# Performance work log

Hardware: AMD Instinct MI355X
Metric: run time of the kernel (lower is better)

The kernel has to match this reference:

```python
import jax, jax.numpy as jnp
import numpy as np

B, S, D = 4, 4096, 1024
DD = 4 * D
N_EXPERTS = 8
CAPACITY = 1.0
LN_EPS = 1e-5


def setup_inputs() -> dict:
    key = jax.random.key(0)
    ks = jax.random.split(key, 8)
    s1 = 1.0 / np.sqrt(D)
    s2 = 1.0 / np.sqrt(DD)
    return {
        "x": jax.random.normal(ks[0], (B, S, D), jnp.float32),
        "gate_w": jax.random.normal(ks[1], (N_EXPERTS, D), jnp.float32) * 0.02,
        "ln_w": jnp.ones((D,), jnp.float32),
        "ln_b": jnp.zeros((D,), jnp.float32),
        "fc1s": jax.random.normal(ks[2], (N_EXPERTS, DD, D), jnp.float32) * s1,
        "b1s": jax.random.normal(ks[3], (N_EXPERTS, DD), jnp.float32) * s1,
        "fc2s": jax.random.normal(ks[4], (N_EXPERTS, D, DD), jnp.float32) * s2,
        "b2s": jax.random.normal(ks[5], (N_EXPERTS, D), jnp.float32) * s2,
    }


def reference(x, gate_w, ln_w, ln_b, fc1s, b1s, fc2s, b2s):
    og_shape = x.shape
    d = og_shape[-1]
    xf = x.reshape(-1, d)                       # (bs, d)
    bs = xf.shape[0]
    n = gate_w.shape[0]
    k = int(bs * CAPACITY) // n                 # static capacity per expert

    # softmax gating over experts
    scores = jax.nn.softmax(xf @ gate_w.T, axis=-1)   # (bs, n)

    # per-expert top-k tokens (column-wise descending sort, take first k)
    vals, idx = jax.lax.top_k(scores.T, k)      # (n, k)
    kept_w = vals.T                              # (k, n)
    kept_idx = idx.T                             # (k, n)
    flat_idx = kept_idx.reshape(-1)              # (k*n,) row-major: k outer, n inner

    # gather selected tokens, layernorm
    y = xf[flat_idx].reshape(k, n, d)            # (k, n, d)
    mu = y.mean(-1, keepdims=True)
    var = ((y - mu) ** 2).mean(-1, keepdims=True)
    y = (y - mu) * jax.lax.rsqrt(var + LN_EPS) * ln_w + ln_b

    # per-expert grouped GEMMs
    h = jnp.einsum('knd,nfd->knf', y, fc1s) + b1s          # (k, n, dd)
    h = jax.nn.gelu(h, approximate=True)                   # tanh gelu
    out = jnp.einsum('knf,ndf->knd', h, fc2s) + b2s        # (k, n, d)

    # weight by gate scores and scatter-add back onto the input tokens
    out = out * kept_w[..., None]
    xf = xf.at[flat_idx].add(out.reshape(k * n, d))
    return xf.reshape(og_shape)
```

## Files before the change

kernel.cpp:

```cpp
#include <hip/hip_runtime.h>

#define TOK  16384
#define NEXP 8
#define DIM  1024
#define DDIM 4096
#define KCAP 2048

typedef float  floatx4 __attribute__((ext_vector_type(4)));
typedef short  shortx8 __attribute__((ext_vector_type(8)));

static __device__ __forceinline__ unsigned short f2bf(float x) {
  unsigned u = __float_as_uint(x);
  return (unsigned short)((u + 0x7fffu + ((u >> 16) & 1u)) >> 16);
}

__global__ __launch_bounds__(256) void cvt_kernel(const float* __restrict__ src,
                                                  unsigned short* __restrict__ dst, int n4) {
  int i = blockIdx.x * 256 + threadIdx.x;
  if (i < n4) {
    float4 v = ((const float4*)src)[i];
    ushort4 o = make_ushort4(f2bf(v.x), f2bf(v.y), f2bf(v.z), f2bf(v.w));
    ((ushort4*)dst)[i] = o;
  }
}

__global__ __launch_bounds__(256) void gate_kernel(const float* __restrict__ x,
                                                   const float* __restrict__ gw,
                                                   float* __restrict__ scores) {
  __shared__ float gws[NEXP * DIM];
  int tid = threadIdx.x;
  for (int i = tid; i < NEXP * DIM / 4; i += 256)
    ((float4*)gws)[i] = ((const float4*)gw)[i];
  __syncthreads();
  int wave = tid >> 6, lane = tid & 63;
  int t = blockIdx.x * 4 + wave;
  const float4* xr = (const float4*)(x + (size_t)t * DIM);
  float4 xv[4];
#pragma unroll
  for (int j = 0; j < 4; ++j) xv[j] = xr[j * 64 + lane];
  float acc[NEXP];
#pragma unroll
  for (int e = 0; e < NEXP; ++e) acc[e] = 0.f;
#pragma unroll
  for (int e = 0; e < NEXP; ++e) {
    const float4* g4 = (const float4*)(gws + e * DIM);
#pragma unroll
    for (int j = 0; j < 4; ++j) {
      float4 g = g4[j * 64 + lane];
      acc[e] += xv[j].x * g.x + xv[j].y * g.y + xv[j].z * g.z + xv[j].w * g.w;
    }
  }
#pragma unroll
  for (int off = 32; off > 0; off >>= 1) {
#pragma unroll
    for (int e = 0; e < NEXP; ++e) acc[e] += __shfl_down(acc[e], off);
  }
  if (lane == 0) {
    float mx = acc[0];
#pragma unroll
    for (int e = 1; e < NEXP; ++e) mx = fmaxf(mx, acc[e]);
    float ex[NEXP], sum = 0.f;
#pragma unroll
    for (int e = 0; e < NEXP; ++e) { ex[e] = expf(acc[e] - mx); sum += ex[e]; }
    float inv = 1.f / sum;
#pragma unroll
    for (int e = 0; e < NEXP; ++e) scores[(size_t)e * TOK + t] = ex[e] * inv;
  }
}

#define TKT 1024
#define TKW (TKT / 64)

__device__ __forceinline__ void walk_suffix(const int* hist, int nbins, int cnt_in,
                                            int tid, int* shOut) {
  if (tid < 64) {
    int lane = tid;
    int cum = 0;
    for (int g = nbins / 64 - 1; g >= 0; --g) {
      int c = hist[g * 64 + lane];
      int s = c;
#pragma unroll
      for (int off = 1; off < 64; off <<= 1) {
        int o = __shfl_down(s, off);
        if (lane + off < 64) s += o;
      }
      int gs = __shfl(s, 0);
      if (cnt_in + cum + gs >= KCAP) {
        unsigned long long m = __ballot(cnt_in + cum + s >= KCAP);
        int l = 63 - __clzll(m);
        int sAt = __shfl(s, l), cAt = __shfl(c, l);
        if (lane == 0) { shOut[0] = g * 64 + l; shOut[1] = cnt_in + cum + sAt - cAt; }
        break;
      }
      cum += gs;
    }
  }
}

__global__ __launch_bounds__(TKT) void topk_kernel(const float* __restrict__ scores,
                                                   int* __restrict__ sel,
                                                   float* __restrict__ selw) {
  int e = blockIdx.x;
  const float* s = scores + (size_t)e * TOK;
  int tid = threadIdx.x, lane = tid & 63, wave = tid >> 6;
  __shared__ int hist[2048];
  __shared__ int shBin[2];
  __shared__ int wsum[TKW];

  for (int i = tid; i < 2048; i += TKT) hist[i] = 0;
  __syncthreads();
  for (int i = tid; i < TOK; i += TKT)
    atomicAdd(&hist[__float_as_uint(s[i]) >> 21], 1);
  __syncthreads();
  walk_suffix(hist, 2048, 0, tid, shBin);
  __syncthreads();
  unsigned bin1 = (unsigned)shBin[0];
  int cab = shBin[1];
  __syncthreads();

  for (int i = tid; i < 2048; i += TKT) hist[i] = 0;
  __syncthreads();
  for (int i = tid; i < TOK; i += TKT) {
    unsigned v = __float_as_uint(s[i]);
    if ((v >> 21) == bin1) atomicAdd(&hist[(v >> 10) & 0x7FFu], 1);
  }
  __syncthreads();
  walk_suffix(hist, 2048, cab, tid, shBin);
  __syncthreads();
  unsigned pre21 = (bin1 << 11) | (unsigned)shBin[0];
  cab = shBin[1];
  __syncthreads();

  for (int i = tid; i < 1024; i += TKT) hist[i] = 0;
  __syncthreads();
  for (int i = tid; i < TOK; i += TKT) {
    unsigned v = __float_as_uint(s[i]);
    if ((v >> 10) == pre21) atomicAdd(&hist[v & 0x3FFu], 1);
  }
  __syncthreads();
  walk_suffix(hist, 1024, cab, tid, shBin);
  __syncthreads();
  unsigned T = (pre21 << 10) | (unsigned)shBin[0];
  int n_gt = shBin[1];
  int need = KCAP - n_gt;

  __shared__ int pos;
  __shared__ int tiebase;
  if (tid == 0) { pos = 0; tiebase = 0; }
  __syncthreads();
  for (int chunk = 0; chunk < TOK; chunk += TKT) {
    int i = chunk + tid;
    unsigned v = __float_as_uint(s[i]);
    if (v > T) {
      int p = atomicAdd(&pos, 1);
      sel[e * KCAP + p]  = i;
      selw[e * KCAP + p] = __uint_as_float(v);
    }
    bool tie = (v == T);
    unsigned long long m = __ballot(tie);
    if (lane == 0) wsum[wave] = __popcll(m);
    __syncthreads();
    int base = tiebase;
    for (int w = 0; w < wave; ++w) base += wsum[w];
    int rank = base + __popcll(m & ((1ull << lane) - 1ull));
    if (tie && rank < need) {
      sel[e * KCAP + n_gt + rank]  = i;
      selw[e * KCAP + n_gt + rank] = __uint_as_float(T);
    }
    __syncthreads();
    if (tid == 0) {
      int tb = 0;
#pragma unroll
      for (int w = 0; w < TKW; ++w) tb += wsum[w];
      tiebase += tb;
    }
    __syncthreads();
  }
}

__global__ __launch_bounds__(256) void gather_ln_kernel(const float* __restrict__ x,
                                                        const int* __restrict__ sel,
                                                        const float* __restrict__ lnw,
                                                        const float* __restrict__ lnb,
                                                        unsigned short* __restrict__ Y) {
  int e = blockIdx.y, i = blockIdx.x;
  int tid = threadIdx.x, lane = tid & 63, wave = tid >> 6;
  int t = sel[e * KCAP + i];
  const float4* xr = (const float4*)(x + (size_t)t * DIM);
  float4 v = xr[tid];
  float s  = v.x + v.y + v.z + v.w;
  float sq = v.x * v.x + v.y * v.y + v.z * v.z + v.w * v.w;
#pragma unroll
  for (int off = 32; off > 0; off >>= 1) { s += __shfl_down(s, off); sq += __shfl_down(sq, off); }
  __shared__ float red[8];
  if (lane == 0) { red[wave] = s; red[4 + wave] = sq; }
  __syncthreads();
  s  = red[0] + red[1] + red[2] + red[3];
  sq = red[4] + red[5] + red[6] + red[7];
  float mu  = s * (1.f / DIM);
  float var = sq * (1.f / DIM) - mu * mu;
  float rs  = rsqrtf(var + 1e-5f);
  float4 w = ((const float4*)lnw)[tid];
  float4 b = ((const float4*)lnb)[tid];
  ushort4 o = make_ushort4(f2bf((v.x - mu) * rs * w.x + b.x),
                           f2bf((v.y - mu) * rs * w.y + b.y),
                           f2bf((v.z - mu) * rs * w.z + b.z),
                           f2bf((v.w - mu) * rs * w.w + b.w));
  ((ushort4*)(Y + ((size_t)e * KCAP + i) * DIM))[tid] = o;
}

#define BM  256
#define BN  256
#define BKT 64
#define HTILE 8192

template <int MODE, int M, int N, int K>
__global__ __launch_bounds__(512, 2) void gemm_kernel(
    const unsigned short* __restrict__ Aall,
    const unsigned short* __restrict__ Ball,
    const float* __restrict__ biasAll,
    unsigned short* __restrict__ Hall,
    float* __restrict__ Out,
    const int* __restrict__ sel, const float* __restrict__ selw) {

  __shared__ __align__(16) unsigned short As[2 * 2 * HTILE];
  __shared__ __align__(16) unsigned short Bs[2 * 2 * HTILE];
  __shared__ int   selS[BM];
  __shared__ float wS[BM];

  int tid = threadIdx.x, lane = tid & 63, wave = tid >> 6;
  int m_w = wave >> 2, n_w = wave & 3;
  int hb  = n_w >> 1, nb0 = (n_w & 1) * 64;
  int row = lane & 15, quad = lane >> 4, r7 = row & 7;
  int r8 = lane >> 3, j8 = lane & 7;

  constexpr int nxt = N >> 8, nyt = M >> 8, per = nxt * nyt;
  constexpr int nwg = per * NEXP;
  int bid = blockIdx.x;
  int swz = (bid & 7) * (nwg >> 3) + (bid >> 3);
  int e   = swz / per;
  int rem = swz - e * per;
  int by  = rem / nxt;
  int bx  = rem - by * nxt;
  int m0 = by * BM, n0 = bx * BN;
  constexpr int NT = K / BKT;

  const unsigned short* A = Aall + (size_t)e * M * K;
  const unsigned short* B = Ball + (size_t)e * N * K;
  const float* bias = biasAll + (size_t)e * N;

  if (MODE == 2 && tid < BM) {
    selS[tid] = sel[e * KCAP + m0 + tid];
    wS[tid]   = selw[e * KCAP + m0 + tid];
  }
  __syncthreads();

#define STAGE(DST, G, RC0, TT, HALF, BUF)                                              \
  do {                                                                                 \
    int tt_ = (TT) < NT ? (TT) : NT - 1;                                               \
    const unsigned short* g_ =                                                         \
        (G) + (size_t)((RC0) + (HALF) * 128 + wave * 16 + r8) * K + tt_ * BKT +        \
        ((j8 ^ r8) << 3);                                                              \
    unsigned short* l_ = (DST) + ((BUF) * 2 + (HALF)) * HTILE + wave * 16 * 64;        \
    __builtin_amdgcn_global_load_lds((const __attribute__((address_space(1))) void*)g_,\
        (__attribute__((address_space(3))) void*)l_, 16, 0, 0);                        \
    __builtin_amdgcn_global_load_lds(                                                  \
        (const __attribute__((address_space(1))) void*)(g_ + (size_t)8 * K),           \
        (__attribute__((address_space(3))) void*)(l_ + 8 * 64), 16, 0, 0);             \
  } while (0)

#define LDA(MQ)                                                                        \
  _Pragma("unroll") for (int ti = 0; ti < 4; ++ti)                                     \
  _Pragma("unroll") for (int kki = 0; kki < 2; ++kki)                                  \
    a[ti][kki] = *(const shortx8*)&As[(cur * 2 + m_w) * HTILE +                        \
        ((MQ) * 64 + ti * 16 + row) * 64 + (((quad + 4 * kki) ^ r7) << 3)];

#define LDB(BREG, NQ)                                                                  \
  _Pragma("unroll") for (int tj = 0; tj < 2; ++tj)                                     \
  _Pragma("unroll") for (int kki = 0; kki < 2; ++kki)                                  \
    BREG[tj][kki] = *(const shortx8*)&Bs[(cur * 2 + hb) * HTILE +                      \
        (nb0 + (NQ) * 32 + tj * 16 + row) * 64 + (((quad + 4 * kki) ^ r7) << 3)];

#define MFMAQ(MQ, BREG, NQ)                                                            \
  _Pragma("unroll") for (int kki = 0; kki < 2; ++kki)                                  \
  _Pragma("unroll") for (int ti = 0; ti < 4; ++ti)                                     \
  _Pragma("unroll") for (int tj = 0; tj < 2; ++tj)                                     \
    acc[(MQ) * 4 + ti][(NQ) * 2 + tj] = __builtin_amdgcn_mfma_f32_16x16x32_bf16(       \
        a[ti][kki], BREG[tj][kki], acc[(MQ) * 4 + ti][(NQ) * 2 + tj], 0, 0, 0);

#define PH_MID()                                                                       \
  __builtin_amdgcn_s_barrier();                                                        \
  asm volatile("s_waitcnt lgkmcnt(0)" ::: "memory");                                   \
  __builtin_amdgcn_s_setprio(1);

#define PH_END()                                                                       \
  __builtin_amdgcn_s_setprio(0);                                                       \
  __builtin_amdgcn_s_barrier();

#define PH_END_VM(NN)                                                                  \
  __builtin_amdgcn_s_setprio(0);                                                       \
  asm volatile("s_waitcnt vmcnt(" #NN ")" ::: "memory");                               \
  __builtin_amdgcn_s_barrier();

  floatx4 acc[8][4];
  floatx4 zero = {0.f, 0.f, 0.f, 0.f};
#pragma unroll
  for (int i = 0; i < 8; ++i)
#pragma unroll
    for (int j = 0; j < 4; ++j) acc[i][j] = zero;

  shortx8 a[4][2], b0[2][2], b1[2][2];

  STAGE(As, A, m0, 0, 0, 0);
  STAGE(Bs, B, n0, 0, 0, 0);
  STAGE(As, A, m0, 0, 1, 0);
  STAGE(Bs, B, n0, 0, 1, 0);
  STAGE(As, A, m0, 1, 0, 1);
  STAGE(Bs, B, n0, 1, 0, 1);
  asm volatile("s_waitcnt vmcnt(4)" ::: "memory");
  __builtin_amdgcn_s_barrier();

  for (int t = 0; t < NT; ++t) {
    int cur = t & 1, nb = cur ^ 1;
    LDA(0); LDB(b0, 0);
    STAGE(As, A, m0, t + 1, 1, nb);
    STAGE(Bs, B, n0, t + 1, 1, nb);
    asm volatile("s_waitcnt lgkmcnt(8)" ::: "memory");
    PH_MID(); MFMAQ(0, b0, 0); PH_END();
    LDB(b1, 1);
    PH_MID(); MFMAQ(0, b1, 1); PH_END();
    LDA(1);
    PH_MID(); MFMAQ(1, b0, 0); PH_END();
    STAGE(As, A, m0, t + 2, 0, cur);
    STAGE(Bs, B, n0, t + 2, 0, cur);
    PH_MID(); MFMAQ(1, b1, 1); PH_END_VM(4);
  }
  asm volatile("s_waitcnt vmcnt(0)" ::: "memory");

#pragma unroll
  for (int ti = 0; ti < 8; ++ti) {
#pragma unroll
    for (int tj = 0; tj < 4; ++tj) {
      int gn = n0 + n_w * 64 + tj * 16 + row;
      float bb = bias[gn];
#pragma unroll
      for (int r = 0; r < 4; ++r) {
        int lrow = m_w * 128 + ti * 16 + quad * 4 + r;
        float v = acc[ti][tj][r] + bb;
        if (MODE == 1) {
          float u = 0.7978845608028654f * (v + 0.044715f * v * v * v);
          u = fminf(u, 15.f);
          float e2 = __expf(2.f * u);
          float th = __fdividef(e2 - 1.f, e2 + 1.f);
          float g = 0.5f * v * (1.f + th);
          Hall[(size_t)e * M * N + (size_t)(m0 + lrow) * N + gn] = f2bf(g);
        } else {
          atomicAdd(&Out[(size_t)selS[lrow] * DIM + gn], wS[lrow] * v);
        }
      }
    }
  }
#undef STAGE
#undef LDA
#undef LDB
#undef MFMAQ
#undef PH_MID
#undef PH_END
#undef PH_END_VM
}

extern "C" void kernel_launch(void* const* d_in, const int* in_sizes, int n_in,
                              void* d_out, int out_size, void* d_ws, size_t ws_size,
                              hipStream_t stream) {
  const float* x   = (const float*)d_in[0];
  const float* gw  = (const float*)d_in[1];
  const float* lnw = (const float*)d_in[2];
  const float* lnb = (const float*)d_in[3];
  const float* fc1 = (const float*)d_in[4];
  const float* b1  = (const float*)d_in[5];
  const float* fc2 = (const float*)d_in[6];
  const float* b2  = (const float*)d_in[7];
  float* out = (float*)d_out;

  char* p = (char*)d_ws;
  float* scores = (float*)p;                 p += (size_t)NEXP * TOK * 4;
  int*   sel    = (int*)p;                   p += (size_t)NEXP * KCAP * 4;
  float* selw   = (float*)p;                 p += (size_t)NEXP * KCAP * 4;
  unsigned short* Wb = (unsigned short*)p;   p += (size_t)NEXP * DDIM * DIM * 2;
  unsigned short* Y  = (unsigned short*)p;   p += (size_t)NEXP * KCAP * DIM * 2;
  unsigned short* H  = (unsigned short*)p;   p += (size_t)NEXP * KCAP * DDIM * 2;

  hipMemcpyAsync(out, x, (size_t)TOK * DIM * sizeof(float), hipMemcpyDeviceToDevice, stream);

  gate_kernel<<<TOK / 4, 256, 0, stream>>>(x, gw, scores);
  topk_kernel<<<NEXP, TKT, 0, stream>>>(scores, sel, selw);
  gather_ln_kernel<<<dim3(KCAP, NEXP), 256, 0, stream>>>(x, sel, lnw, lnb, Y);

  const int n4w = NEXP * DDIM * DIM / 4;
  cvt_kernel<<<n4w / 256, 256, 0, stream>>>(fc1, Wb, n4w);
  gemm_kernel<1, KCAP, DDIM, DIM><<<dim3((DDIM / BN) * (KCAP / BM) * NEXP), 512, 0, stream>>>(
      Y, Wb, b1, H, nullptr, nullptr, nullptr);

  cvt_kernel<<<n4w / 256, 256, 0, stream>>>(fc2, Wb, n4w);
  gemm_kernel<2, KCAP, DIM, DDIM><<<dim3((DIM / BN) * (KCAP / BM) * NEXP), 512, 0, stream>>>(
      H, Wb, b2, nullptr, out, sel, selw);
}
```

Baseline: 826.8 us.

## Fold input copy into gate kernel and reschedule GEMM prefetch stages

The gate kernel now writes the input rows straight to the output buffer, which removes the separate device-to-device memcpy. The GEMM prefetch order changes so the B tile for step t+1 is issued in two halves interleaved between MFMA phases, with the waitcnt thresholds adjusted to match. The MFMA loop order moves kki innermost. M/N/K become runtime arguments instead of template constants, which may cost some compile-time constant folding of index math and the K-loop trip count. The new waitcnt accounting is fragile and could open a race if the counts no longer match the outstanding loads.

```diff
diff --git a/kernel.cpp b/kernel.cpp
--- a/kernel.cpp
+++ b/kernel.cpp
@@ -26,7 +26,8 @@
 
 __global__ __launch_bounds__(256) void gate_kernel(const float* __restrict__ x,
                                                    const float* __restrict__ gw,
-                                                   float* __restrict__ scores) {
+                                                   float* __restrict__ scores,
+                                                   float* __restrict__ out) {
   __shared__ float gws[NEXP * DIM];
   int tid = threadIdx.x;
   for (int i = tid; i < NEXP * DIM / 4; i += 256)
@@ -38,6 +39,9 @@
   float4 xv[4];
 #pragma unroll
   for (int j = 0; j < 4; ++j) xv[j] = xr[j * 64 + lane];
+  float4* orow = (float4*)(out + (size_t)t * DIM);
+#pragma unroll
+  for (int j = 0; j < 4; ++j) orow[j * 64 + lane] = xv[j];
   float acc[NEXP];
 #pragma unroll
   for (int e = 0; e < NEXP; ++e) acc[e] = 0.f;
@@ -214,11 +218,12 @@
 #define BKT 64
 #define HTILE 8192
 
-template <int MODE, int M, int N, int K>
+template <int MODE>
 __global__ __launch_bounds__(512, 2) void gemm_kernel(
     const unsigned short* __restrict__ Aall,
     const unsigned short* __restrict__ Ball,
     const float* __restrict__ biasAll,
+    int M, int N, int K,
     unsigned short* __restrict__ Hall,
     float* __restrict__ Out,
     const int* __restrict__ sel, const float* __restrict__ selw) {
@@ -234,8 +239,8 @@
   int row = lane & 15, quad = lane >> 4, r7 = row & 7;
   int r8 = lane >> 3, j8 = lane & 7;
 
-  constexpr int nxt = N >> 8, nyt = M >> 8, per = nxt * nyt;
-  constexpr int nwg = per * NEXP;
+  int nxt = N >> 8, nyt = M >> 8, per = nxt * nyt;
+  int nwg = per * NEXP;
   int bid = blockIdx.x;
   int swz = (bid & 7) * (nwg >> 3) + (bid >> 3);
   int e   = swz / per;
@@ -243,7 +248,7 @@
   int by  = rem / nxt;
   int bx  = rem - by * nxt;
   int m0 = by * BM, n0 = bx * BN;
-  constexpr int NT = K / BKT;
+  int NT = K / BKT;
 
   const unsigned short* A = Aall + (size_t)e * M * K;
   const unsigned short* B = Ball + (size_t)e * N * K;
@@ -282,9 +287,9 @@
         (nb0 + (NQ) * 32 + tj * 16 + row) * 64 + (((quad + 4 * kki) ^ r7) << 3)];
 
 #define MFMAQ(MQ, BREG, NQ)                                                            \
-  _Pragma("unroll") for (int kki = 0; kki < 2; ++kki)                                  \
   _Pragma("unroll") for (int ti = 0; ti < 4; ++ti)                                     \
   _Pragma("unroll") for (int tj = 0; tj < 2; ++tj)                                     \
+  _Pragma("unroll") for (int kki = 0; kki < 2; ++kki)                                  \
     acc[(MQ) * 4 + ti][(NQ) * 2 + tj] = __builtin_amdgcn_mfma_f32_16x16x32_bf16(       \
         a[ti][kki], BREG[tj][kki], acc[(MQ) * 4 + ti][(NQ) * 2 + tj], 0, 0, 0);
 
@@ -297,9 +302,9 @@
   __builtin_amdgcn_s_setprio(0);                                                       \
   __builtin_amdgcn_s_barrier();
 
-#define PH_END_VM(NN)                                                                  \
+#define PH_END_VM()                                                                    \
   __builtin_amdgcn_s_setprio(0);                                                       \
-  asm volatile("s_waitcnt vmcnt(" #NN ")" ::: "memory");                               \
+  asm volatile("s_waitcnt vmcnt(2)" ::: "memory");                                     \
   __builtin_amdgcn_s_barrier();
 
   floatx4 acc[8][4];
@@ -312,28 +317,27 @@
   shortx8 a[4][2], b0[2][2], b1[2][2];
 
   STAGE(As, A, m0, 0, 0, 0);
+  STAGE(As, A, m0, 0, 1, 0);
   STAGE(Bs, B, n0, 0, 0, 0);
-  STAGE(As, A, m0, 0, 1, 0);
   STAGE(Bs, B, n0, 0, 1, 0);
   STAGE(As, A, m0, 1, 0, 1);
-  STAGE(Bs, B, n0, 1, 0, 1);
-  asm volatile("s_waitcnt vmcnt(4)" ::: "memory");
+  asm volatile("s_waitcnt vmcnt(2)" ::: "memory");
   __builtin_amdgcn_s_barrier();
 
   for (int t = 0; t < NT; ++t) {
     int cur = t & 1, nb = cur ^ 1;
     LDA(0); LDB(b0, 0);
     STAGE(As, A, m0, t + 1, 1, nb);
-    STAGE(Bs, B, n0, t + 1, 1, nb);
     asm volatile("s_waitcnt lgkmcnt(8)" ::: "memory");
     PH_MID(); MFMAQ(0, b0, 0); PH_END();
     LDB(b1, 1);
+    STAGE(Bs, B, n0, t + 1, 0, nb);
     PH_MID(); MFMAQ(0, b1, 1); PH_END();
     LDA(1);
+    STAGE(Bs, B, n0, t + 1, 1, nb);
     PH_MID(); MFMAQ(1, b0, 0); PH_END();
     STAGE(As, A, m0, t + 2, 0, cur);
-    STAGE(Bs, B, n0, t + 2, 0, cur);
-    PH_MID(); MFMAQ(1, b1, 1); PH_END_VM(4);
+    PH_MID(); MFMAQ(1, b1, 1); PH_END_VM();
   }
   asm volatile("s_waitcnt vmcnt(0)" ::: "memory");
 
@@ -390,18 +394,16 @@
   unsigned short* Y  = (unsigned short*)p;   p += (size_t)NEXP * KCAP * DIM * 2;
   unsigned short* H  = (unsigned short*)p;   p += (size_t)NEXP * KCAP * DDIM * 2;
 
-  hipMemcpyAsync(out, x, (size_t)TOK * DIM * sizeof(float), hipMemcpyDeviceToDevice, stream);
-
-  gate_kernel<<<TOK / 4, 256, 0, stream>>>(x, gw, scores);
+  gate_kernel<<<TOK / 4, 256, 0, stream>>>(x, gw, scores, out);
   topk_kernel<<<NEXP, TKT, 0, stream>>>(scores, sel, selw);
   gather_ln_kernel<<<dim3(KCAP, NEXP), 256, 0, stream>>>(x, sel, lnw, lnb, Y);
 
   const int n4w = NEXP * DDIM * DIM / 4;
   cvt_kernel<<<n4w / 256, 256, 0, stream>>>(fc1, Wb, n4w);
-  gemm_kernel<1, KCAP, DDIM, DIM><<<dim3((DDIM / BN) * (KCAP / BM) * NEXP), 512, 0, stream>>>(
-      Y, Wb, b1, H, nullptr, nullptr, nullptr);
+  gemm_kernel<1><<<dim3((DDIM / BN) * (KCAP / BM) * NEXP), 512, 0, stream>>>(
+      Y, Wb, b1, KCAP, DDIM, DIM, H, nullptr, nullptr, nullptr);
 
   cvt_kernel<<<n4w / 256, 256, 0, stream>>>(fc2, Wb, n4w);
-  gemm_kernel<2, KCAP, DIM, DDIM><<<dim3((DIM / BN) * (KCAP / BM) * NEXP), 512, 0, stream>>>(
-      H, Wb, b2, nullptr, out, sel, selw);
-}
+  gemm_kernel<2><<<dim3((DIM / BN) * (KCAP / BM) * NEXP), 512, 0, stream>>>(
+      H, Wb, b2, KCAP, DIM, DDIM, nullptr, out, sel, selw);
+}
```

New measurement: 767.2 us. -7.2%, faster.
